# Kernel optimization log

Hardware: AMD Instinct MI355X
Metric: run time of the kernel (lower is better)

Reference implementation:

```python
import jax, jax.numpy as jnp
import numpy as np
from jax import lax

D_MODEL = 1024
FFN = 4096
CHUNK = 256
TTT_LR = 0.01
KSIZE = 5


def setup_inputs() -> dict:
    key = jax.random.key(0)
    ks = jax.random.split(key, 7)
    B, T = 2, 4096
    x = jax.random.normal(ks[0], (B, T, D_MODEL), dtype=jnp.float32)
    ttt_target = jax.random.normal(ks[1], (B, T, D_MODEL), dtype=jnp.float32)
    w_gate_up = jax.random.normal(ks[2], (2 * FFN, D_MODEL), dtype=jnp.float32) * 0.02
    w_down = jax.random.normal(ks[3], (D_MODEL, FFN), dtype=jnp.float32) * 0.02
    ttt_proj = jax.random.normal(ks[4], (D_MODEL, D_MODEL), dtype=jnp.float32) * 0.02
    conv_w = jax.random.normal(ks[5], (D_MODEL, 1, KSIZE), dtype=jnp.float32) * 0.02
    conv_b = jax.random.normal(ks[6], (D_MODEL,), dtype=jnp.float32) * 0.02
    return {"x": x, "ttt_target": ttt_target, "w_gate_up": w_gate_up,
            "w_down": w_down, "ttt_proj": ttt_proj, "conv_w": conv_w, "conv_b": conv_b}


def _pad_and_chunk(a, chunk):
    B, T, D = a.shape
    pad = (-T) % chunk
    if pad:
        a = jnp.pad(a, ((0, 0), (0, pad), (0, 0)))
    return a.reshape(B, -1, chunk, D)


def reference(x, ttt_target, w_gate_up, w_down, ttt_proj, conv_w, conv_b):
    B, T, D = x.shape
    # SwiGLU up path
    gate_up = jnp.einsum('btd,fd->btf', x, w_gate_up)  # (B,T,2F)
    gate, up = jnp.split(gate_up, 2, axis=-1)
    h = jax.nn.silu(gate) * up  # (B,T,F)
    # causal depthwise conv on ttt_target (torch pads K-1 both sides then slices [:T])
    t_ncl = ttt_target.transpose(0, 2, 1)  # (B,D,T)
    t = lax.conv_general_dilated(
        t_ncl, conv_w, window_strides=(1,), padding=[(KSIZE - 1, 0)],
        dimension_numbers=('NCH', 'OIH', 'NCH'), feature_group_count=D)
    t = (t + conv_b[None, :, None]).transpose(0, 2, 1)  # (B,T,D)
    # chunk
    h_c = _pad_and_chunk(h, CHUNK)  # (B,nc,C,F)
    t_c = _pad_and_chunk(t, CHUNK)  # (B,nc,C,D)
    nc = h_c.shape[1]
    if nc > 1:
        t_proj = jnp.einsum('btcd,ed->btce', t_c[:, :-1], ttt_proj)  # (B,nc-1,C,D)
        d_down = jnp.einsum('btch,btcd->btdh', h_c[:, :-1], t_proj)  # (B,nc-1,D,F)
    else:
        d_down = jnp.zeros((B, 0, D, FFN), dtype=h.dtype)
    w_orig = jnp.broadcast_to(w_down[None, None], (B, 1, D, FFN))
    w_all = jnp.concatenate([w_orig, d_down * jnp.float32(TTT_LR)], axis=1)
    w_adapted = jnp.cumsum(w_all, axis=1)  # (B,nc,D,F)
    out = jnp.einsum('btdh,btch->btcd', w_adapted, h_c)  # (B,nc,C,D)
    return out.reshape(B, -1, D)[:, :T]
```

## Files before the change

kernel.cpp:

```cpp
#include <hip/hip_runtime.h>
#include <hip/hip_bf16.h>
#include <stdint.h>

typedef unsigned short ushort_t;
typedef __bf16 bf16x8 __attribute__((ext_vector_type(8)));
typedef float f32x16 __attribute__((ext_vector_type(16)));

#define BM 128
#define BN 128
#define BK 64

__device__ inline float b2f(ushort_t u) {
    unsigned int x = ((unsigned int)u) << 16;
    float f; __builtin_memcpy(&f, &x, 4); return f;
}
__device__ inline ushort_t f2b(float f) {
    unsigned int x; __builtin_memcpy(&x, &f, 4);
    unsigned int r = (x + 0x7FFFu + ((x >> 16) & 1u)) >> 16;
    return (ushort_t)r;
}
__device__ inline void stage16(const ushort_t* g, ushort_t* s) {
    __builtin_amdgcn_global_load_lds((const __attribute__((address_space(1))) void*)g,
                                     (__attribute__((address_space(3))) void*)s, 16, 0, 0);
}
__device__ inline int swz(int r) { return (r & 7) ^ ((r >> 3) & 3); }
__device__ inline void stage_tile(const ushort_t* G, int ld, int k0, ushort_t* S, int tid) {
#pragma unroll
    for (int t = 0; t < 4; ++t) {
        int e = tid + t * 256;
        int row = e >> 3;
        int sw = ((e & 7) ^ swz(row)) * 8;
        stage16(G + (long long)row * ld + k0 + sw, &S[e * 8]);
    }
}
__device__ inline bf16x8 ldfrag(const ushort_t* S, int r, int c) {
    return *(const bf16x8*)&S[r * BK + ((c ^ swz(r)) * 8)];
}
__device__ inline void tile_decode(int& m0, int& n0) {
    const int nx = gridDim.x;
    int lin = blockIdx.y * nx + blockIdx.x;
    if ((nx & 7) == 0) {
        int q = nx >> 3;
        int k = lin & 7, s = lin >> 3;
        n0 = (k * q + s % q) * BN;
        m0 = (s / q) * BM;
    } else {
        m0 = blockIdx.y * BM;
        n0 = blockIdx.x * BN;
    }
}


#define SBAR() __builtin_amdgcn_sched_barrier(0)
#define BARRIER() do { SBAR(); __builtin_amdgcn_s_barrier(); SBAR(); } while (0)
#define WAITV(N) asm volatile("s_waitcnt vmcnt(" #N ")" ::: "memory")

__device__ inline int sw2(int r) { return ((r) & 3) ^ ((r >> 3) & 3); }

__device__ inline void stage_half(const ushort_t* G, int ldg, int kElem,
                                  ushort_t* Sbuf, int tid) {
#pragma unroll
    for (int i2 = 0; i2 < 2; ++i2) {
        int s = tid + i2 * 512;
        int r = s >> 2, q = s & 3;
        int c = q ^ sw2(r);
        stage16(G + (long long)r * ldg + kElem + c * 8, Sbuf + s * 8);
    }
}
__device__ inline void stage_halfA(const ushort_t* G, int ldg, ushort_t* Sbuf, int tid) {
    int r = tid >> 2, q = tid & 3;
    int c = q ^ sw2(r);
    stage16(G + (long long)r * ldg + c * 8, Sbuf + tid * 8);
}
__device__ inline int frag_off(int r, int c) {
    return r * 32 + ((c ^ sw2(r)) & 3) * 8;
}

__device__ __forceinline__ void gemm256_core(const ushort_t* __restrict__ Ag, int lda,
                                             const ushort_t* __restrict__ Bg, int ldb,
                                             int K, ushort_t* smem, int tid,
                                             int wr, int wc, int l32, int hl,
                                             f32x16 (&acc)[4][2]) {
    const int NH = K >> 5;
    ushort_t* Ab0 = smem;
    ushort_t* Bb0 = smem + 32768;

    int oa[4][2], ob[2][2];
#pragma unroll
    for (int m2 = 0; m2 < 4; ++m2)
#pragma unroll
        for (int k2 = 0; k2 < 2; ++k2)
            oa[m2][k2] = frag_off(wr * 128 + m2 * 32 + l32, k2 * 2 + hl);
#pragma unroll
    for (int n2 = 0; n2 < 2; ++n2)
#pragma unroll
        for (int k2 = 0; k2 < 2; ++k2)
            ob[n2][k2] = frag_off(wc * 64 + n2 * 32 + l32, k2 * 2 + hl);

    stage_half(Ag, lda, 0,  Ab0,          tid);
    stage_half(Bg, ldb, 0,  Bb0,          tid);
    stage_half(Ag, lda, 32, Ab0 + 8192,   tid);
    stage_half(Bg, ldb, 32, Bb0 + 8192,   tid);
    stage_half(Ag, lda, 64, Ab0 + 16384,  tid);
    stage_half(Bg, ldb, 64, Bb0 + 16384,  tid);
    WAITV(8);
    BARRIER();

    int h = 0;
    for (; h < NH - 3; ++h) {
        ushort_t* cA = Ab0 + (h & 3) * 8192;
        ushort_t* cB = Bb0 + (h & 3) * 8192;
        int nb = (h + 3) & 3;
        stage_half(Ag, lda, (h + 3) << 5, Ab0 + nb * 8192, tid);
        stage_half(Bg, ldb, (h + 3) << 5, Bb0 + nb * 8192, tid);
        bf16x8 af_[4][2], bf_[2][2];
#pragma unroll
        for (int k2 = 0; k2 < 2; ++k2) {
#pragma unroll
            for (int m2 = 0; m2 < 4; ++m2)
                af_[m2][k2] = *(const bf16x8*)&cA[oa[m2][k2]];
#pragma unroll
            for (int n2 = 0; n2 < 2; ++n2)
                bf_[n2][k2] = *(const bf16x8*)&cB[ob[n2][k2]];
        }
        __builtin_amdgcn_s_setprio(1);
#pragma unroll
        for (int k2 = 0; k2 < 2; ++k2)
#pragma unroll
            for (int m2 = 0; m2 < 4; ++m2)
#pragma unroll
                for (int n2 = 0; n2 < 2; ++n2)
                    acc[m2][n2] = __builtin_amdgcn_mfma_f32_32x32x16_bf16(
                        af_[m2][k2], bf_[n2][k2], acc[m2][n2], 0, 0, 0);
        __builtin_amdgcn_s_setprio(0);
        WAITV(8);
        BARRIER();
    }
    for (; h < NH; ++h) {
        ushort_t* cA = Ab0 + (h & 3) * 8192;
        ushort_t* cB = Bb0 + (h & 3) * 8192;
        bf16x8 af_[4][2], bf_[2][2];
#pragma unroll
        for (int k2 = 0; k2 < 2; ++k2) {
#pragma unroll
            for (int m2 = 0; m2 < 4; ++m2)
                af_[m2][k2] = *(const bf16x8*)&cA[oa[m2][k2]];
#pragma unroll
            for (int n2 = 0; n2 < 2; ++n2)
                bf_[n2][k2] = *(const bf16x8*)&cB[ob[n2][k2]];
        }
        __builtin_amdgcn_s_setprio(1);
#pragma unroll
        for (int k2 = 0; k2 < 2; ++k2)
#pragma unroll
            for (int m2 = 0; m2 < 4; ++m2)
#pragma unroll
                for (int n2 = 0; n2 < 2; ++n2)
                    acc[m2][n2] = __builtin_amdgcn_mfma_f32_32x32x16_bf16(
                        af_[m2][k2], bf_[n2][k2], acc[m2][n2], 0, 0, 0);
        __builtin_amdgcn_s_setprio(0);
        if (h + 2 < NH) { WAITV(4); } else { WAITV(0); }
        BARRIER();
    }
}

__global__ __launch_bounds__(512, 2)
void k_gemm256_silu(const ushort_t* __restrict__ A, const ushort_t* __restrict__ Bp,
                    ushort_t* __restrict__ H) {
    extern __shared__ __attribute__((aligned(16))) ushort_t smem2[];
    const int tid = threadIdx.x;
    const int lane = tid & 63, l32 = lane & 31, hl = lane >> 5;
    const int wv = tid >> 6, wr = wv >> 2, wc = wv & 3;
    int lin = blockIdx.y * 32 + blockIdx.x;
    int k8 = lin & 7, s = lin >> 3;
    int n0 = (k8 * 4 + (s & 3)) * 256;
    int m0 = (s >> 2) * 256;
    const ushort_t* Ag = A + (long long)m0 * 1024;
    const ushort_t* Bg = Bp + (long long)n0 * 1024;
    f32x16 acc[4][2];
#pragma unroll
    for (int i = 0; i < 4; ++i) { acc[i][0] = (f32x16)(0.f); acc[i][1] = (f32x16)(0.f); }
    gemm256_core(Ag, 1024, Bg, 1024, 1024, smem2, tid, wr, wc, l32, hl, acc);
    const int hc = (n0 >> 1) + wc * 32 + l32;
#pragma unroll
    for (int mi = 0; mi < 4; ++mi)
#pragma unroll
        for (int reg = 0; reg < 16; ++reg) {
            int row = m0 + wr * 128 + mi * 32 + (reg & 3) + 8 * (reg >> 2) + 4 * hl;
            float g = acc[mi][0][reg], u = acc[mi][1][reg];
            float sg = g / (1.f + __expf(-g));
            H[(long long)row * 4096 + hc] = f2b(sg * u);
        }
}

__global__ __launch_bounds__(512, 2)
void k_gemm256_tri(const ushort_t* __restrict__ Hh, ushort_t* __restrict__ P) {
    extern __shared__ __attribute__((aligned(16))) ushort_t smem2[];
    const int tid = threadIdx.x;
    const int lane = tid & 63, l32 = lane & 31, hl = lane >> 5;
    const int wv = tid >> 6, wr = wv >> 2, wc = wv & 3;
    int pairIdx = (blockIdx.x & 7) * 30 + (blockIdx.x >> 3);
    const int bb = pairIdx / 120;
    int p = pairIdx % 120;
    int i = 1, rem = p;
    while (rem >= i) { rem -= i; ++i; }
    const int j = rem;
    const ushort_t* Ag = Hh + (long long)bb * 4096 * 4096 + (long long)(i * 256) * 4096;
    const ushort_t* Bg = Hh + (long long)bb * 4096 * 4096 + (long long)(j * 256) * 4096;
    f32x16 acc[4][2];
#pragma unroll
    for (int a = 0; a < 4; ++a) { acc[a][0] = (f32x16)(0.f); acc[a][1] = (f32x16)(0.f); }
    gemm256_core(Ag, 4096, Bg, 4096, 4096, smem2, tid, wr, wc, l32, hl, acc);
    ushort_t* Pp = P + (long long)bb * 4096 * 4096;
#pragma unroll
    for (int mi = 0; mi < 4; ++mi)
#pragma unroll
        for (int nj = 0; nj < 2; ++nj) {
            int col = j * 256 + wc * 64 + nj * 32 + l32;
#pragma unroll
            for (int reg = 0; reg < 16; ++reg) {
                int row = i * 256 + wr * 128 + mi * 32 + (reg & 3) + 8 * (reg >> 2) + 4 * hl;
                Pp[(long long)row * 4096 + col] = f2b(acc[mi][nj][reg]);
            }
        }
}

__global__ __launch_bounds__(512, 2)
void k_gemm256_out(const ushort_t* __restrict__ h, const ushort_t* __restrict__ wdown,
                   const ushort_t* __restrict__ P, const ushort_t* __restrict__ tpT,
                   float* __restrict__ out) {
    constexpr int T = 4096, D = 1024, F = 4096, C = 256, K1 = 4096;
    extern __shared__ __attribute__((aligned(16))) ushort_t smem2[];
    const int tid = threadIdx.x;
    const int lane = tid & 63, l32 = lane & 31, hl = lane >> 5;
    const int wv = tid >> 6, wr = wv >> 2, wc = wv & 3;

    const int bx = blockIdx.x;
    const int logical = (bx & 7) * 32 + (bx >> 3);
    const int z = logical >> 3, t = logical & 7;
    const int bb = z >> 4, ii = z & 15;
    const int m0 = (t >> 2) * 128, n0 = (t & 3) * 256;
    const int K = K1 + ii * C;
    const int NH = K >> 5;

    const ushort_t* hA = h + (long long)bb * T * F + (long long)(ii * C + m0) * F;
    const ushort_t* pA = P + (long long)bb * T * T + (long long)(ii * C + m0) * T;
    const ushort_t* wB = wdown + (long long)n0 * F;
    const ushort_t* tB = tpT + (long long)bb * D * T + (long long)n0 * T;

    ushort_t* Ab0 = smem2;
    ushort_t* Bb0 = smem2 + 16384;

    int oa[2][2], ob[2][2];
#pragma unroll
    for (int m2 = 0; m2 < 2; ++m2)
#pragma unroll
        for (int k2 = 0; k2 < 2; ++k2)
            oa[m2][k2] = frag_off(wr * 64 + m2 * 32 + l32, k2 * 2 + hl);
#pragma unroll
    for (int n2 = 0; n2 < 2; ++n2)
#pragma unroll
        for (int k2 = 0; k2 < 2; ++k2)
            ob[n2][k2] = frag_off(wc * 64 + n2 * 32 + l32, k2 * 2 + hl);

    f32x16 acc[2][2];
#pragma unroll
    for (int a = 0; a < 2; ++a)
#pragma unroll
        for (int c = 0; c < 2; ++c) acc[a][c] = (f32x16)(0.f);

    auto srcA = [&](int kE) { return kE < K1 ? hA + kE : pA + (kE - K1); };
    auto srcB = [&](int kE) { return kE < K1 ? wB + kE : tB + (kE - K1); };

    stage_halfA(srcA(0),  F, Ab0,         tid);
    stage_half (srcB(0),  F, 0, Bb0,      tid);
    stage_halfA(srcA(32), F, Ab0 + 4096,  tid);
    stage_half (srcB(32), F, 0, Bb0 + 8192, tid);
    stage_halfA(srcA(64), F, Ab0 + 8192,  tid);
    stage_half (srcB(64), F, 0, Bb0 + 16384, tid);
    WAITV(6);
    BARRIER();

    int hh = 0;
    for (; hh < NH - 3; ++hh) {
        ushort_t* cA = Ab0 + (hh & 3) * 4096;
        ushort_t* cB = Bb0 + (hh & 3) * 8192;
        int nb = (hh + 3) & 3;
        stage_halfA(srcA((hh + 3) << 5), F, Ab0 + nb * 4096, tid);
        stage_half (srcB((hh + 3) << 5), F, 0, Bb0 + nb * 8192, tid);
        bf16x8 af_[2][2], bf_[2][2];
#pragma unroll
        for (int k2 = 0; k2 < 2; ++k2) {
#pragma unroll
            for (int m2 = 0; m2 < 2; ++m2)
                af_[m2][k2] = *(const bf16x8*)&cA[oa[m2][k2]];
#pragma unroll
            for (int n2 = 0; n2 < 2; ++n2)
                bf_[n2][k2] = *(const bf16x8*)&cB[ob[n2][k2]];
        }
        __builtin_amdgcn_s_setprio(1);
#pragma unroll
        for (int k2 = 0; k2 < 2; ++k2)
#pragma unroll
            for (int m2 = 0; m2 < 2; ++m2)
#pragma unroll
                for (int n2 = 0; n2 < 2; ++n2)
                    acc[m2][n2] = __builtin_amdgcn_mfma_f32_32x32x16_bf16(
                        af_[m2][k2], bf_[n2][k2], acc[m2][n2], 0, 0, 0);
        __builtin_amdgcn_s_setprio(0);
        WAITV(6);
        BARRIER();
    }
    for (; hh < NH; ++hh) {
        ushort_t* cA = Ab0 + (hh & 3) * 4096;
        ushort_t* cB = Bb0 + (hh & 3) * 8192;
        bf16x8 af_[2][2], bf_[2][2];
#pragma unroll
        for (int k2 = 0; k2 < 2; ++k2) {
#pragma unroll
            for (int m2 = 0; m2 < 2; ++m2)
                af_[m2][k2] = *(const bf16x8*)&cA[oa[m2][k2]];
#pragma unroll
            for (int n2 = 0; n2 < 2; ++n2)
                bf_[n2][k2] = *(const bf16x8*)&cB[ob[n2][k2]];
        }
        __builtin_amdgcn_s_setprio(1);
#pragma unroll
        for (int k2 = 0; k2 < 2; ++k2)
#pragma unroll
            for (int m2 = 0; m2 < 2; ++m2)
#pragma unroll
                for (int n2 = 0; n2 < 2; ++n2)
                    acc[m2][n2] = __builtin_amdgcn_mfma_f32_32x32x16_bf16(
                        af_[m2][k2], bf_[n2][k2], acc[m2][n2], 0, 0, 0);
        __builtin_amdgcn_s_setprio(0);
        if (hh + 2 < NH) { WAITV(3); } else { WAITV(0); }
        BARRIER();
    }

    float* Op = out + (long long)bb * T * D + (long long)(ii * C) * D;
#pragma unroll
    for (int mi = 0; mi < 2; ++mi)
#pragma unroll
        for (int nj = 0; nj < 2; ++nj) {
            int col = n0 + wc * 64 + nj * 32 + l32;
#pragma unroll
            for (int reg = 0; reg < 16; ++reg) {
                int row = m0 + wr * 64 + mi * 32 + (reg & 3) + 8 * (reg >> 2) + 4 * hl;
                Op[(long long)row * D + col] = acc[mi][nj][reg];
            }
        }
}

__global__ void k_prep(const float* __restrict__ x, const float* __restrict__ wgu,
                       const float* __restrict__ proj, const float* __restrict__ wdown,
                       const float* __restrict__ tt, const float* __restrict__ cw,
                       const float* __restrict__ cb,
                       ushort_t* __restrict__ xb, ushort_t* __restrict__ gb,
                       ushort_t* __restrict__ pb, ushort_t* __restrict__ wb,
                       ushort_t* __restrict__ tb, int permW) {
    constexpr int T = 4096, D = 1024;
    int blk = blockIdx.x;
    if (blk < 21504) {
        int i = blk * 256 + threadIdx.x;
        const float* src; ushort_t* dst; int off; int dstoff;
        if (i < 2097152)      { src = x;     dst = xb; off = i; dstoff = off; }
        else if (i < 4194304) {
            src = wgu; dst = gb; off = i - 2097152;
            if (permW) {
                int r = off >> 8, cu = off & 255;
                int pr = (r < 4096) ? (((r >> 5) << 6) + (r & 31))
                                    : ((((r - 4096) >> 5) << 6) + 32 + ((r - 4096) & 31));
                dstoff = (pr << 8) + cu;
            } else dstoff = off;
        }
        else if (i < 4456448) { src = proj;  dst = pb; off = i - 4194304; dstoff = off; }
        else                  { src = wdown; dst = wb; off = i - 4456448; dstoff = off; }
        float4 v = ((const float4*)src)[off];
        ushort4 o; o.x = f2b(v.x); o.y = f2b(v.y); o.z = f2b(v.z); o.w = f2b(v.w);
        ((ushort4*)dst)[dstoff] = o;
    } else {
        int idx = (blk - 21504) * 256 + threadIdx.x;
        int d = idx & (D - 1);
        int tq = (idx >> 10) & (T / 4 - 1);
        int b = idx / (D * (T / 4));
        int t0 = tq * 4;
        const float* base = tt + (long long)b * T * D + d;
        float w0 = cw[d * 5 + 0], w1 = cw[d * 5 + 1], w2 = cw[d * 5 + 2],
              w3 = cw[d * 5 + 3], w4 = cw[d * 5 + 4];
        float bias = cb[d];
        float win[8];
#pragma unroll
        for (int m = 0; m < 8; ++m) {
            int ts = t0 - 4 + m;
            win[m] = (ts >= 0) ? base[(long long)ts * D] : 0.f;
        }
        ushort_t* op = tb + (long long)b * T * D + (long long)t0 * D + d;
#pragma unroll
        for (int r = 0; r < 4; ++r) {
            float a = bias + w0 * win[r] + w1 * win[r + 1] + w2 * win[r + 2]
                    + w3 * win[r + 3] + w4 * win[r + 4];
            op[(long long)r * D] = f2b(a);
        }
    }
}

__global__ __launch_bounds__(256, 4)
void k_gemm_nt(const ushort_t* __restrict__ A, const ushort_t* __restrict__ B,
               ushort_t* __restrict__ C, int K, int lda, int ldb, int ldc,
               long long sAb, long long sBb, long long sCb, float scale) {
    __shared__ __attribute__((aligned(16))) ushort_t sA[BM * BK];
    __shared__ __attribute__((aligned(16))) ushort_t sB[BN * BK];

    int m0, n0;
    tile_decode(m0, n0);
    const int bb = blockIdx.z;
    const ushort_t* Ab = A + bb * sAb + (long long)m0 * lda;
    const ushort_t* Bb = B + bb * sBb + (long long)n0 * ldb;

    const int tid = threadIdx.x;
    const int lane = tid & 63, l32 = lane & 31, half = lane >> 5;
    const int wave = tid >> 6;
    const int wm = (wave >> 1) * 64, wn = (wave & 1) * 64;

    f32x16 acc[2][2];
#pragma unroll
    for (int i = 0; i < 2; ++i)
#pragma unroll
        for (int j = 0; j < 2; ++j) acc[i][j] = (f32x16)(0.f);

    for (int k0 = 0; k0 < K; k0 += BK) {
        __syncthreads();
        stage_tile(Ab, lda, k0, sA, tid);
        stage_tile(Bb, ldb, k0, sB, tid);
        __syncthreads();
#pragma unroll
        for (int ks = 0; ks < 4; ++ks) {
            bf16x8 af[2], bfr[2];
#pragma unroll
            for (int mi = 0; mi < 2; ++mi)
                af[mi] = ldfrag(sA, wm + mi * 32 + l32, ks * 2 + half);
#pragma unroll
            for (int nj = 0; nj < 2; ++nj)
                bfr[nj] = ldfrag(sB, wn + nj * 32 + l32, ks * 2 + half);
#pragma unroll
            for (int mi = 0; mi < 2; ++mi)
#pragma unroll
                for (int nj = 0; nj < 2; ++nj)
                    acc[mi][nj] = __builtin_amdgcn_mfma_f32_32x32x16_bf16(af[mi], bfr[nj], acc[mi][nj], 0, 0, 0);
        }
    }

    ushort_t* Cp = C + bb * sCb;
#pragma unroll
    for (int mi = 0; mi < 2; ++mi)
#pragma unroll
        for (int nj = 0; nj < 2; ++nj) {
            int col = n0 + wn + nj * 32 + l32;
#pragma unroll
            for (int reg = 0; reg < 16; ++reg) {
                int row = m0 + wm + mi * 32 + (reg & 3) + 8 * (reg >> 2) + 4 * half;
                Cp[(long long)row * ldc + col] = f2b(acc[mi][nj][reg] * scale);
            }
        }
}

__global__ __launch_bounds__(256)
void k_gemm_silu(const ushort_t* __restrict__ A, const ushort_t* __restrict__ Bg,
                 const ushort_t* __restrict__ Bu, ushort_t* __restrict__ H,
                 int K, int lda, int ldb, int ldh) {
    __shared__ __attribute__((aligned(16))) ushort_t sA[BM * BK];
    __shared__ __attribute__((aligned(16))) ushort_t sBg[BN * BK];
    __shared__ __attribute__((aligned(16))) ushort_t sBu[BN * BK];

    int m0, n0;
    tile_decode(m0, n0);
    const ushort_t* Ab = A + (long long)m0 * lda;
    const ushort_t* Bgb = Bg + (long long)n0 * ldb;
    const ushort_t* Bub = Bu + (long long)n0 * ldb;

    const int tid = threadIdx.x;
    const int lane = tid & 63, l32 = lane & 31, half = lane >> 5;
    const int wave = tid >> 6;
    const int wm = (wave >> 1) * 64, wn = (wave & 1) * 64;

    f32x16 ag[2][2], au[2][2];
#pragma unroll
    for (int i = 0; i < 2; ++i)
#pragma unroll
        for (int j = 0; j < 2; ++j) { ag[i][j] = (f32x16)(0.f); au[i][j] = (f32x16)(0.f); }

    for (int k0 = 0; k0 < K; k0 += BK) {
        __syncthreads();
        stage_tile(Ab, lda, k0, sA, tid);
        stage_tile(Bgb, ldb, k0, sBg, tid);
        stage_tile(Bub, ldb, k0, sBu, tid);
        __syncthreads();
#pragma unroll
        for (int ks = 0; ks < 4; ++ks) {
            bf16x8 af[2], bg[2], bu[2];
#pragma unroll
            for (int mi = 0; mi < 2; ++mi)
                af[mi] = ldfrag(sA, wm + mi * 32 + l32, ks * 2 + half);
#pragma unroll
            for (int nj = 0; nj < 2; ++nj) {
                bg[nj] = ldfrag(sBg, wn + nj * 32 + l32, ks * 2 + half);
                bu[nj] = ldfrag(sBu, wn + nj * 32 + l32, ks * 2 + half);
            }
#pragma unroll
            for (int mi = 0; mi < 2; ++mi)
#pragma unroll
                for (int nj = 0; nj < 2; ++nj) {
                    ag[mi][nj] = __builtin_amdgcn_mfma_f32_32x32x16_bf16(af[mi], bg[nj], ag[mi][nj], 0, 0, 0);
                    au[mi][nj] = __builtin_amdgcn_mfma_f32_32x32x16_bf16(af[mi], bu[nj], au[mi][nj], 0, 0, 0);
                }
        }
    }

#pragma unroll
    for (int mi = 0; mi < 2; ++mi)
#pragma unroll
        for (int nj = 0; nj < 2; ++nj) {
            int col = n0 + wn + nj * 32 + l32;
#pragma unroll
            for (int reg = 0; reg < 16; ++reg) {
                int row = m0 + wm + mi * 32 + (reg & 3) + 8 * (reg >> 2) + 4 * half;
                float g = ag[mi][nj][reg], u = au[mi][nj][reg];
                float s = g / (1.f + __expf(-g));
                H[(long long)row * ldh + col] = f2b(s * u);
            }
        }
}

__global__ __launch_bounds__(256, 4)
void k_gemm_tri(const ushort_t* __restrict__ H, ushort_t* __restrict__ P,
                int K, int ldh, int ldp, long long sHb, long long sPb) {
    __shared__ __attribute__((aligned(16))) ushort_t sA[BM * BK];
    __shared__ __attribute__((aligned(16))) ushort_t sB[BN * BK];

    const int lin = blockIdx.x;
    const int g = lin >> 5, w = lin & 31;
    const int xk = w & 7, t = w >> 3;
    int pairIdx = g * 8 + xk;
    const int bb = pairIdx / 120;
    int p = pairIdx % 120;
    int i = 1, rem = p;
    while (rem >= i) { rem -= i; ++i; }
    const int j = rem;
    const int m0 = (t >> 1) * BM, n0 = (t & 1) * BN;

    const ushort_t* Ab = H + bb * sHb + (long long)(i * 256 + m0) * ldh;
    const ushort_t* Bb = H + bb * sHb + (long long)(j * 256 + n0) * ldh;

    const int tid = threadIdx.x;
    const int lane = tid & 63, l32 = lane & 31, half = lane >> 5;
    const int wave = tid >> 6;
    const int wm = (wave >> 1) * 64, wn = (wave & 1) * 64;

    f32x16 acc[2][2];
#pragma unroll
    for (int a = 0; a < 2; ++a)
#pragma unroll
        for (int c = 0; c < 2; ++c) acc[a][c] = (f32x16)(0.f);

    for (int k0 = 0; k0 < K; k0 += BK) {
        __syncthreads();
        stage_tile(Ab, ldh, k0, sA, tid);
        stage_tile(Bb, ldh, k0, sB, tid);
        __syncthreads();
#pragma unroll
        for (int ks = 0; ks < 4; ++ks) {
            bf16x8 af[2], bfr[2];
#pragma unroll
            for (int mi = 0; mi < 2; ++mi)
                af[mi] = ldfrag(sA, wm + mi * 32 + l32, ks * 2 + half);
#pragma unroll
            for (int nj = 0; nj < 2; ++nj)
                bfr[nj] = ldfrag(sB, wn + nj * 32 + l32, ks * 2 + half);
#pragma unroll
            for (int mi = 0; mi < 2; ++mi)
#pragma unroll
                for (int nj = 0; nj < 2; ++nj)
                    acc[mi][nj] = __builtin_amdgcn_mfma_f32_32x32x16_bf16(af[mi], bfr[nj], acc[mi][nj], 0, 0, 0);
        }
    }

    ushort_t* Pp = P + bb * sPb;
#pragma unroll
    for (int mi = 0; mi < 2; ++mi)
#pragma unroll
        for (int nj = 0; nj < 2; ++nj) {
            int col = j * 256 + n0 + wn + nj * 32 + l32;
#pragma unroll
            for (int reg = 0; reg < 16; ++reg) {
                int row = i * 256 + m0 + wm + mi * 32 + (reg & 3) + 8 * (reg >> 2) + 4 * half;
                Pp[(long long)row * ldp + col] = f2b(acc[mi][nj][reg]);
            }
        }
}

__global__ __launch_bounds__(256, 4)
void k_gemm_out(const ushort_t* __restrict__ h, const ushort_t* __restrict__ wdown,
                const ushort_t* __restrict__ P, const ushort_t* __restrict__ tpT,
                float* __restrict__ out) {
    constexpr int T = 4096, D = 1024, F = 4096, C = 256, K1 = 4096;
    __shared__ __attribute__((aligned(16))) ushort_t sA[BM * BK];
    __shared__ __attribute__((aligned(16))) ushort_t sB[BN * BK];

    const int z = blockIdx.z, bb = z >> 4, ii = z & 15;
    const int K2 = ii * C;
    int m0, n0;
    tile_decode(m0, n0);

    const ushort_t* A1 = h + (long long)bb * T * F + (long long)(ii * C + m0) * F;
    const ushort_t* B1 = wdown + (long long)n0 * F;
    const ushort_t* A2 = P + (long long)bb * T * T + (long long)(ii * C + m0) * T;
    const ushort_t* B2 = tpT + (long long)bb * D * T + (long long)n0 * T;

    const int tid = threadIdx.x;
    const int lane = tid & 63, l32 = lane & 31, half = lane >> 5;
    const int wave = tid >> 6;
    const int wm = (wave >> 1) * 64, wn = (wave & 1) * 64;

    f32x16 acc[2][2];
#pragma unroll
    for (int i = 0; i < 2; ++i)
#pragma unroll
        for (int j = 0; j < 2; ++j) acc[i][j] = (f32x16)(0.f);

    const int K = K1 + K2;
    for (int k0 = 0; k0 < K; k0 += BK) {
        const ushort_t* As = (k0 < K1) ? A1 + k0 : A2 + (k0 - K1);
        const ushort_t* Bs = (k0 < K1) ? B1 + k0 : B2 + (k0 - K1);
        __syncthreads();
        stage_tile(As, 4096, 0, sA, tid);
        stage_tile(Bs, 4096, 0, sB, tid);
        __syncthreads();
#pragma unroll
        for (int ks = 0; ks < 4; ++ks) {
            bf16x8 af[2], bfr[2];
#pragma unroll
            for (int mi = 0; mi < 2; ++mi)
                af[mi] = ldfrag(sA, wm + mi * 32 + l32, ks * 2 + half);
#pragma unroll
            for (int nj = 0; nj < 2; ++nj)
                bfr[nj] = ldfrag(sB, wn + nj * 32 + l32, ks * 2 + half);
#pragma unroll
            for (int mi = 0; mi < 2; ++mi)
#pragma unroll
                for (int nj = 0; nj < 2; ++nj)
                    acc[mi][nj] = __builtin_amdgcn_mfma_f32_32x32x16_bf16(af[mi], bfr[nj], acc[mi][nj], 0, 0, 0);
        }
    }

    float* Op = out + (long long)bb * T * D + (long long)ii * C * D;
#pragma unroll
    for (int mi = 0; mi < 2; ++mi)
#pragma unroll
        for (int nj = 0; nj < 2; ++nj) {
            int col = n0 + wn + nj * 32 + l32;
#pragma unroll
            for (int reg = 0; reg < 16; ++reg) {
                int row = m0 + wm + mi * 32 + (reg & 3) + 8 * (reg >> 2) + 4 * half;
                Op[(long long)row * D + col] = acc[mi][nj][reg];
            }
        }
}

static int g_big = -1;

extern "C" void kernel_launch(void* const* d_in, const int* in_sizes, int n_in,
                              void* d_out, int out_size, void* d_ws, size_t ws_size,
                              hipStream_t stream) {
    const float* x         = (const float*)d_in[0];
    const float* ttt_tgt   = (const float*)d_in[1];
    const float* w_gate_up = (const float*)d_in[2];
    const float* w_down    = (const float*)d_in[3];
    const float* ttt_proj  = (const float*)d_in[4];
    const float* conv_w    = (const float*)d_in[5];
    const float* conv_b    = (const float*)d_in[6];
    float* out = (float*)d_out;
    (void)in_sizes; (void)n_in; (void)out_size; (void)ws_size;

    constexpr int Bb = 2, T = 4096, D = 1024, F = 4096, C = 256;
    constexpr float LR = 0.01f;

    if (g_big < 0) {
        hipError_t e1 = hipFuncSetAttribute((const void*)k_gemm256_silu,
                                            hipFuncAttributeMaxDynamicSharedMemorySize, 131072);
        hipError_t e2 = hipFuncSetAttribute((const void*)k_gemm256_tri,
                                            hipFuncAttributeMaxDynamicSharedMemorySize, 131072);
        hipError_t e3 = hipFuncSetAttribute((const void*)k_gemm256_out,
                                            hipFuncAttributeMaxDynamicSharedMemorySize, 98304);
        g_big = (e1 == hipSuccess && e2 == hipSuccess && e3 == hipSuccess) ? 1 : 0;
    }

    char* ws = (char*)d_ws;
    ushort_t* x_bf     = (ushort_t*)(ws);
    ushort_t* wgu_bf   = (ushort_t*)(ws + 16777216LL);
    ushort_t* t_bf     = (ushort_t*)(ws + 2 * 16777216LL);
    ushort_t* P        = (ushort_t*)(ws);
    ushort_t* proj_bf  = (ushort_t*)(ws + 67108864LL);
    ushort_t* wdown_bf = (ushort_t*)(ws + 67108864LL + 2097152LL);
    ushort_t* tpT      = (ushort_t*)(ws + 67108864LL + 2097152LL + 8388608LL);
    ushort_t* h        = (ushort_t*)(ws + 67108864LL + 2097152LL + 8388608LL + 16777216LL);

    k_prep<<<21504 + 8192, 256, 0, stream>>>(x, w_gate_up, ttt_proj, w_down,
                                             ttt_tgt, conv_w, conv_b,
                                             x_bf, wgu_bf, proj_bf, wdown_bf, t_bf, g_big);

    k_gemm_nt<<<dim3(T / BN, D / BM, Bb), 256, 0, stream>>>(
        proj_bf, t_bf, tpT, D, D, D, T,
        0, (long long)T * D, (long long)D * T, LR);

    if (g_big) {
        k_gemm256_silu<<<dim3(32, 32, 1), 512, 131072, stream>>>(x_bf, wgu_bf, h);
    } else {
        k_gemm_silu<<<dim3(F / BN, (Bb * T) / BM, 1), 256, 0, stream>>>(
            x_bf, wgu_bf, wgu_bf + (long long)F * D, h, D, D, D, F);
    }

    if (g_big) {
        k_gemm256_tri<<<dim3(240, 1, 1), 512, 131072, stream>>>(h, P);
    } else {
        k_gemm_tri<<<dim3(960, 1, 1), 256, 0, stream>>>(
            h, P, F, F, T, (long long)T * F, (long long)T * T);
    }

    if (g_big) {
        k_gemm256_out<<<dim3(256, 1, 1), 512, 98304, stream>>>(h, wdown_bf, P, tpT, out);
    } else {
        k_gemm_out<<<dim3(D / BN, C / BM, Bb * 16), 256, 0, stream>>>(
            h, wdown_bf, P, tpT, out);
    }
}
```

Measured before the change: 563.7 us.

## Use 16-wave blocks for big GEMMs and split-K balance the output GEMM

The 256x256 silu and triangular GEMM kernels now run 1024 threads (16 waves), each wave owning a 64x64 sub-tile. They use a double-buffered two-half staging pipeline over BK=64 in place of the 4-stage ring of 32-wide K slices. The output GEMM pairs chunk i with chunk 15-i and splits each chunk's K range in half, accumulating into a zeroed output with atomicAdd, to even out the triangular work across blocks. This adds a memset, fp32 atomic traffic and nondeterministic summation order, and the 1024-thread path is enabled only when the attribute query confirms support.

Measured after the change: 608.5 us. 8.0% more time.

```diff
diff --git a/kernel.cpp b/kernel.cpp
--- a/kernel.cpp
+++ b/kernel.cpp
@@ -57,67 +57,75 @@
 
 __device__ inline int sw2(int r) { return ((r) & 3) ^ ((r >> 3) & 3); }
 
-__device__ inline void stage_half(const ushort_t* G, int ldg, int kElem,
-                                  ushort_t* Sbuf, int tid) {
+__device__ inline void stage1k(const ushort_t* G, int ldg, int kElem,
+                               ushort_t* Sbuf, int tid) {
+    int r = tid >> 2, q = tid & 3;
+    int c = q ^ sw2(r);
+    stage16(G + (long long)r * ldg + kElem + c * 8, Sbuf + tid * 8);
+}
+__device__ inline void ostageA(const ushort_t* G, ushort_t* Sbuf, int tid) {
+    int r = tid >> 2, q = tid & 3;
+    stage16(G + (long long)r * 4096 + (q ^ sw2(r)) * 8, Sbuf + tid * 8);
+}
+__device__ inline void ostageB(const ushort_t* G, ushort_t* Sbuf, int tid) {
 #pragma unroll
     for (int i2 = 0; i2 < 2; ++i2) {
         int s = tid + i2 * 512;
         int r = s >> 2, q = s & 3;
-        int c = q ^ sw2(r);
-        stage16(G + (long long)r * ldg + kElem + c * 8, Sbuf + s * 8);
-    }
-}
-__device__ inline void stage_halfA(const ushort_t* G, int ldg, ushort_t* Sbuf, int tid) {
-    int r = tid >> 2, q = tid & 3;
-    int c = q ^ sw2(r);
-    stage16(G + (long long)r * ldg + c * 8, Sbuf + tid * 8);
+        stage16(G + (long long)r * 4096 + (q ^ sw2(r)) * 8, Sbuf + s * 8);
+    }
 }
 __device__ inline int frag_off(int r, int c) {
     return r * 32 + ((c ^ sw2(r)) & 3) * 8;
 }
 
-__device__ __forceinline__ void gemm256_core(const ushort_t* __restrict__ Ag, int lda,
-                                             const ushort_t* __restrict__ Bg, int ldb,
-                                             int K, ushort_t* smem, int tid,
-                                             int wr, int wc, int l32, int hl,
-                                             f32x16 (&acc)[4][2]) {
-    const int NH = K >> 5;
-    ushort_t* Ab0 = smem;
-    ushort_t* Bb0 = smem + 32768;
-
-    int oa[4][2], ob[2][2];
-#pragma unroll
-    for (int m2 = 0; m2 < 4; ++m2)
+__device__ __forceinline__ void gemm256w16_core(const ushort_t* __restrict__ Ag, int lda,
+                                                const ushort_t* __restrict__ Bg, int ldb,
+                                                int K, ushort_t* smem, int tid,
+                                                int wr, int wc, int l32, int hl,
+                                                f32x16 (&acc)[2][2]) {
+    ushort_t* A0s = smem;
+    ushort_t* A1s = smem + 16384;
+    ushort_t* B0s = smem + 32768;
+    ushort_t* B1s = smem + 49152;
+    const int NT = K >> 6;
+
+    int oa[2][2], ob[2][2];
+#pragma unroll
+    for (int m2 = 0; m2 < 2; ++m2)
 #pragma unroll
         for (int k2 = 0; k2 < 2; ++k2)
-            oa[m2][k2] = frag_off(wr * 128 + m2 * 32 + l32, k2 * 2 + hl);
+            oa[m2][k2] = frag_off(wr * 64 + m2 * 32 + l32, k2 * 2 + hl);
 #pragma unroll
     for (int n2 = 0; n2 < 2; ++n2)
 #pragma unroll
         for (int k2 = 0; k2 < 2; ++k2)
             ob[n2][k2] = frag_off(wc * 64 + n2 * 32 + l32, k2 * 2 + hl);
 
-    stage_half(Ag, lda, 0,  Ab0,          tid);
-    stage_half(Bg, ldb, 0,  Bb0,          tid);
-    stage_half(Ag, lda, 32, Ab0 + 8192,   tid);
-    stage_half(Bg, ldb, 32, Bb0 + 8192,   tid);
-    stage_half(Ag, lda, 64, Ab0 + 16384,  tid);
-    stage_half(Bg, ldb, 64, Bb0 + 16384,  tid);
-    WAITV(8);
+    stage1k(Ag, lda, 0,  A0s,        tid);
+    stage1k(Bg, ldb, 0,  B0s,        tid);
+    stage1k(Ag, lda, 32, A0s + 8192, tid);
+    stage1k(Bg, ldb, 32, B0s + 8192, tid);
+    stage1k(Ag, lda, 64, A1s,        tid);
+    stage1k(Bg, ldb, 64, B1s,        tid);
+    WAITV(4);
     BARRIER();
 
-    int h = 0;
-    for (; h < NH - 3; ++h) {
-        ushort_t* cA = Ab0 + (h & 3) * 8192;
-        ushort_t* cB = Bb0 + (h & 3) * 8192;
-        int nb = (h + 3) & 3;
-        stage_half(Ag, lda, (h + 3) << 5, Ab0 + nb * 8192, tid);
-        stage_half(Bg, ldb, (h + 3) << 5, Bb0 + nb * 8192, tid);
-        bf16x8 af_[4][2], bf_[2][2];
+    for (int kt = 0; kt < NT; ++kt) {
+        ushort_t* cA = (kt & 1) ? A1s : A0s;
+        ushort_t* cB = (kt & 1) ? B1s : B0s;
+        ushort_t* nA = (kt & 1) ? A0s : A1s;
+        ushort_t* nB = (kt & 1) ? B0s : B1s;
+        const bool h1 = (kt + 1 < NT), h2 = (kt + 2 < NT);
+        bf16x8 af_[2][2], bf_[2][2];
+        if (h1) {
+            stage1k(Ag, lda, ((kt + 1) << 6) + 32, nA + 8192, tid);
+            stage1k(Bg, ldb, ((kt + 1) << 6) + 32, nB + 8192, tid);
+        }
 #pragma unroll
         for (int k2 = 0; k2 < 2; ++k2) {
 #pragma unroll
-            for (int m2 = 0; m2 < 4; ++m2)
+            for (int m2 = 0; m2 < 2; ++m2)
                 af_[m2][k2] = *(const bf16x8*)&cA[oa[m2][k2]];
 #pragma unroll
             for (int n2 = 0; n2 < 2; ++n2)
@@ -127,44 +135,43 @@
 #pragma unroll
         for (int k2 = 0; k2 < 2; ++k2)
 #pragma unroll
-            for (int m2 = 0; m2 < 4; ++m2)
+            for (int m2 = 0; m2 < 2; ++m2)
 #pragma unroll
                 for (int n2 = 0; n2 < 2; ++n2)
                     acc[m2][n2] = __builtin_amdgcn_mfma_f32_32x32x16_bf16(
                         af_[m2][k2], bf_[n2][k2], acc[m2][n2], 0, 0, 0);
         __builtin_amdgcn_s_setprio(0);
-        WAITV(8);
+        if (h1) { WAITV(4); } else { WAITV(0); }
         BARRIER();
-    }
-    for (; h < NH; ++h) {
-        ushort_t* cA = Ab0 + (h & 3) * 8192;
-        ushort_t* cB = Bb0 + (h & 3) * 8192;
-        bf16x8 af_[4][2], bf_[2][2];
+        if (h2) {
+            stage1k(Ag, lda, (kt + 2) << 6, cA, tid);
+            stage1k(Bg, ldb, (kt + 2) << 6, cB, tid);
+        }
 #pragma unroll
         for (int k2 = 0; k2 < 2; ++k2) {
 #pragma unroll
-            for (int m2 = 0; m2 < 4; ++m2)
-                af_[m2][k2] = *(const bf16x8*)&cA[oa[m2][k2]];
+            for (int m2 = 0; m2 < 2; ++m2)
+                af_[m2][k2] = *(const bf16x8*)&cA[oa[m2][k2] + 8192];
 #pragma unroll
             for (int n2 = 0; n2 < 2; ++n2)
-                bf_[n2][k2] = *(const bf16x8*)&cB[ob[n2][k2]];
+                bf_[n2][k2] = *(const bf16x8*)&cB[ob[n2][k2] + 8192];
         }
         __builtin_amdgcn_s_setprio(1);
 #pragma unroll
         for (int k2 = 0; k2 < 2; ++k2)
 #pragma unroll
-            for (int m2 = 0; m2 < 4; ++m2)
+            for (int m2 = 0; m2 < 2; ++m2)
 #pragma unroll
                 for (int n2 = 0; n2 < 2; ++n2)
                     acc[m2][n2] = __builtin_amdgcn_mfma_f32_32x32x16_bf16(
                         af_[m2][k2], bf_[n2][k2], acc[m2][n2], 0, 0, 0);
         __builtin_amdgcn_s_setprio(0);
-        if (h + 2 < NH) { WAITV(4); } else { WAITV(0); }
+        if (h1) { if (h2) { WAITV(4); } else { WAITV(2); } } else { WAITV(0); }
         BARRIER();
     }
 }
 
-__global__ __launch_bounds__(512, 2)
+__global__ __launch_bounds__(1024, 4)
 void k_gemm256_silu(const ushort_t* __restrict__ A, const ushort_t* __restrict__ Bp,
                     ushort_t* __restrict__ H) {
     extern __shared__ __attribute__((aligned(16))) ushort_t smem2[];
@@ -177,23 +184,23 @@
     int m0 = (s >> 2) * 256;
     const ushort_t* Ag = A + (long long)m0 * 1024;
     const ushort_t* Bg = Bp + (long long)n0 * 1024;
-    f32x16 acc[4][2];
-#pragma unroll
-    for (int i = 0; i < 4; ++i) { acc[i][0] = (f32x16)(0.f); acc[i][1] = (f32x16)(0.f); }
-    gemm256_core(Ag, 1024, Bg, 1024, 1024, smem2, tid, wr, wc, l32, hl, acc);
+    f32x16 acc[2][2];
+#pragma unroll
+    for (int i = 0; i < 2; ++i) { acc[i][0] = (f32x16)(0.f); acc[i][1] = (f32x16)(0.f); }
+    gemm256w16_core(Ag, 1024, Bg, 1024, 1024, smem2, tid, wr, wc, l32, hl, acc);
     const int hc = (n0 >> 1) + wc * 32 + l32;
 #pragma unroll
-    for (int mi = 0; mi < 4; ++mi)
+    for (int mi = 0; mi < 2; ++mi)
 #pragma unroll
         for (int reg = 0; reg < 16; ++reg) {
-            int row = m0 + wr * 128 + mi * 32 + (reg & 3) + 8 * (reg >> 2) + 4 * hl;
+            int row = m0 + wr * 64 + mi * 32 + (reg & 3) + 8 * (reg >> 2) + 4 * hl;
             float g = acc[mi][0][reg], u = acc[mi][1][reg];
             float sg = g / (1.f + __expf(-g));
             H[(long long)row * 4096 + hc] = f2b(sg * u);
         }
 }
 
-__global__ __launch_bounds__(512, 2)
+__global__ __launch_bounds__(1024, 4)
 void k_gemm256_tri(const ushort_t* __restrict__ Hh, ushort_t* __restrict__ P) {
     extern __shared__ __attribute__((aligned(16))) ushort_t smem2[];
     const int tid = threadIdx.x;
@@ -207,19 +214,19 @@
     const int j = rem;
     const ushort_t* Ag = Hh + (long long)bb * 4096 * 4096 + (long long)(i * 256) * 4096;
     const ushort_t* Bg = Hh + (long long)bb * 4096 * 4096 + (long long)(j * 256) * 4096;
-    f32x16 acc[4][2];
-#pragma unroll
-    for (int a = 0; a < 4; ++a) { acc[a][0] = (f32x16)(0.f); acc[a][1] = (f32x16)(0.f); }
-    gemm256_core(Ag, 4096, Bg, 4096, 4096, smem2, tid, wr, wc, l32, hl, acc);
+    f32x16 acc[2][2];
+#pragma unroll
+    for (int a = 0; a < 2; ++a) { acc[a][0] = (f32x16)(0.f); acc[a][1] = (f32x16)(0.f); }
+    gemm256w16_core(Ag, 4096, Bg, 4096, 4096, smem2, tid, wr, wc, l32, hl, acc);
     ushort_t* Pp = P + (long long)bb * 4096 * 4096;
 #pragma unroll
-    for (int mi = 0; mi < 4; ++mi)
+    for (int mi = 0; mi < 2; ++mi)
 #pragma unroll
         for (int nj = 0; nj < 2; ++nj) {
             int col = j * 256 + wc * 64 + nj * 32 + l32;
 #pragma unroll
             for (int reg = 0; reg < 16; ++reg) {
-                int row = i * 256 + wr * 128 + mi * 32 + (reg & 3) + 8 * (reg >> 2) + 4 * hl;
+                int row = i * 256 + wr * 64 + mi * 32 + (reg & 3) + 8 * (reg >> 2) + 4 * hl;
                 Pp[(long long)row * 4096 + col] = f2b(acc[mi][nj][reg]);
             }
         }
@@ -236,20 +243,17 @@
     const int wv = tid >> 6, wr = wv >> 2, wc = wv & 3;
 
     const int bx = blockIdx.x;
-    const int logical = (bx & 7) * 32 + (bx >> 3);
-    const int z = logical >> 3, t = logical & 7;
-    const int bb = z >> 4, ii = z & 15;
+    const int xcd = bx & 7, s = bx >> 3;
+    const int pl = s >> 4, halfSel = (s >> 3) & 1, t = s & 7;
+    const int p = 2 * xcd + pl;
+    const int bb = p >> 3, iiL = p & 7;
+    const int ii0 = halfSel ? (15 - iiL) : iiL;
     const int m0 = (t >> 2) * 128, n0 = (t & 3) * 256;
-    const int K = K1 + ii * C;
-    const int NH = K >> 5;
-
-    const ushort_t* hA = h + (long long)bb * T * F + (long long)(ii * C + m0) * F;
-    const ushort_t* pA = P + (long long)bb * T * T + (long long)(ii * C + m0) * T;
-    const ushort_t* wB = wdown + (long long)n0 * F;
-    const ushort_t* tB = tpT + (long long)bb * D * T + (long long)n0 * T;
-
-    ushort_t* Ab0 = smem2;
-    ushort_t* Bb0 = smem2 + 16384;
+
+    ushort_t* A0s = smem2;
+    ushort_t* A1s = smem2 + 8192;
+    ushort_t* B0s = smem2 + 16384;
+    ushort_t* B1s = smem2 + 32768;
 
     int oa[2][2], ob[2][2];
 #pragma unroll
@@ -263,93 +267,110 @@
         for (int k2 = 0; k2 < 2; ++k2)
             ob[n2][k2] = frag_off(wc * 64 + n2 * 32 + l32, k2 * 2 + hl);
 
-    f32x16 acc[2][2];
-#pragma unroll
-    for (int a = 0; a < 2; ++a)
-#pragma unroll
-        for (int c = 0; c < 2; ++c) acc[a][c] = (f32x16)(0.f);
-
-    auto srcA = [&](int kE) { return kE < K1 ? hA + kE : pA + (kE - K1); };
-    auto srcB = [&](int kE) { return kE < K1 ? wB + kE : tB + (kE - K1); };
-
-    stage_halfA(srcA(0),  F, Ab0,         tid);
-    stage_half (srcB(0),  F, 0, Bb0,      tid);
-    stage_halfA(srcA(32), F, Ab0 + 4096,  tid);
-    stage_half (srcB(32), F, 0, Bb0 + 8192, tid);
-    stage_halfA(srcA(64), F, Ab0 + 8192,  tid);
-    stage_half (srcB(64), F, 0, Bb0 + 16384, tid);
-    WAITV(6);
-    BARRIER();
-
-    int hh = 0;
-    for (; hh < NH - 3; ++hh) {
-        ushort_t* cA = Ab0 + (hh & 3) * 4096;
-        ushort_t* cB = Bb0 + (hh & 3) * 8192;
-        int nb = (hh + 3) & 3;
-        stage_halfA(srcA((hh + 3) << 5), F, Ab0 + nb * 4096, tid);
-        stage_half (srcB((hh + 3) << 5), F, 0, Bb0 + nb * 8192, tid);
-        bf16x8 af_[2][2], bf_[2][2];
-#pragma unroll
-        for (int k2 = 0; k2 < 2; ++k2) {
-#pragma unroll
-            for (int m2 = 0; m2 < 2; ++m2)
-                af_[m2][k2] = *(const bf16x8*)&cA[oa[m2][k2]];
-#pragma unroll
-            for (int n2 = 0; n2 < 2; ++n2)
-                bf_[n2][k2] = *(const bf16x8*)&cB[ob[n2][k2]];
-        }
-        __builtin_amdgcn_s_setprio(1);
-#pragma unroll
-        for (int k2 = 0; k2 < 2; ++k2)
-#pragma unroll
-            for (int m2 = 0; m2 < 2; ++m2)
-#pragma unroll
-                for (int n2 = 0; n2 < 2; ++n2)
-                    acc[m2][n2] = __builtin_amdgcn_mfma_f32_32x32x16_bf16(
-                        af_[m2][k2], bf_[n2][k2], acc[m2][n2], 0, 0, 0);
-        __builtin_amdgcn_s_setprio(0);
+#pragma unroll 1
+    for (int it = 0; it < 2; ++it) {
+        const int ii = it ? (15 - ii0) : ii0;
+        const int NT = 64 + 4 * ii;
+        const int NTh = NT >> 1;
+        const int ktBeg = it ? NTh : 0;
+        const int NTs = it ? (NT - NTh) : NTh;
+
+        const ushort_t* hA = h + (long long)bb * T * F + (long long)(ii * C + m0) * F;
+        const ushort_t* pA = P + (long long)bb * T * T + (long long)(ii * C + m0) * T;
+        const ushort_t* wB = wdown + (long long)n0 * F;
+        const ushort_t* tB = tpT + (long long)bb * D * T + (long long)n0 * T;
+        auto srcA = [&](int kE) { return kE < K1 ? hA + kE : pA + (kE - K1); };
+        auto srcB = [&](int kE) { return kE < K1 ? wB + kE : tB + (kE - K1); };
+
+        f32x16 acc[2][2];
+#pragma unroll
+        for (int a = 0; a < 2; ++a)
+#pragma unroll
+            for (int c = 0; c < 2; ++c) acc[a][c] = (f32x16)(0.f);
+
+        const int kE0 = ktBeg << 6;
+        ostageA(srcA(kE0),      A0s,        tid);
+        ostageB(srcB(kE0),      B0s,        tid);
+        ostageA(srcA(kE0 + 32), A0s + 4096, tid);
+        ostageB(srcB(kE0 + 32), B0s + 8192, tid);
+        ostageA(srcA(kE0 + 64), A1s,        tid);
+        ostageB(srcB(kE0 + 64), B1s,        tid);
         WAITV(6);
         BARRIER();
-    }
-    for (; hh < NH; ++hh) {
-        ushort_t* cA = Ab0 + (hh & 3) * 4096;
-        ushort_t* cB = Bb0 + (hh & 3) * 8192;
-        bf16x8 af_[2][2], bf_[2][2];
-#pragma unroll
-        for (int k2 = 0; k2 < 2; ++k2) {
-#pragma unroll
-            for (int m2 = 0; m2 < 2; ++m2)
-                af_[m2][k2] = *(const bf16x8*)&cA[oa[m2][k2]];
-#pragma unroll
-            for (int n2 = 0; n2 < 2; ++n2)
-                bf_[n2][k2] = *(const bf16x8*)&cB[ob[n2][k2]];
-        }
-        __builtin_amdgcn_s_setprio(1);
-#pragma unroll
-        for (int k2 = 0; k2 < 2; ++k2)
-#pragma unroll
-            for (int m2 = 0; m2 < 2; ++m2)
+
+        for (int kt = 0; kt < NTs; ++kt) {
+            ushort_t* cA = (kt & 1) ? A1s : A0s;
+            ushort_t* cB = (kt & 1) ? B1s : B0s;
+            ushort_t* nA = (kt & 1) ? A0s : A1s;
+            ushort_t* nB = (kt & 1) ? B0s : B1s;
+            const bool h1 = (kt + 1 < NTs), h2 = (kt + 2 < NTs);
+            const int kE1 = (ktBeg + kt + 1) << 6, kE2 = (ktBeg + kt + 2) << 6;
+            bf16x8 af_[2][2], bf_[2][2];
+            if (h1) {
+                ostageA(srcA(kE1 + 32), nA + 4096, tid);
+                ostageB(srcB(kE1 + 32), nB + 8192, tid);
+            }
+#pragma unroll
+            for (int k2 = 0; k2 < 2; ++k2) {
+#pragma unroll
+                for (int m2 = 0; m2 < 2; ++m2)
+                    af_[m2][k2] = *(const bf16x8*)&cA[oa[m2][k2]];
 #pragma unroll
                 for (int n2 = 0; n2 < 2; ++n2)
-                    acc[m2][n2] = __builtin_amdgcn_mfma_f32_32x32x16_bf16(
-                        af_[m2][k2], bf_[n2][k2], acc[m2][n2], 0, 0, 0);
-        __builtin_amdgcn_s_setprio(0);
-        if (hh + 2 < NH) { WAITV(3); } else { WAITV(0); }
-        BARRIER();
-    }
-
-    float* Op = out + (long long)bb * T * D + (long long)(ii * C) * D;
-#pragma unroll
-    for (int mi = 0; mi < 2; ++mi)
-#pragma unroll
-        for (int nj = 0; nj < 2; ++nj) {
-            int col = n0 + wc * 64 + nj * 32 + l32;
-#pragma unroll
-            for (int reg = 0; reg < 16; ++reg) {
-                int row = m0 + wr * 64 + mi * 32 + (reg & 3) + 8 * (reg >> 2) + 4 * hl;
-                Op[(long long)row * D + col] = acc[mi][nj][reg];
-            }
-        }
+                    bf_[n2][k2] = *(const bf16x8*)&cB[ob[n2][k2]];
+            }
+            __builtin_amdgcn_s_setprio(1);
+#pragma unroll
+            for (int k2 = 0; k2 < 2; ++k2)
+#pragma unroll
+                for (int m2 = 0; m2 < 2; ++m2)
+#pragma unroll
+                    for (int n2 = 0; n2 < 2; ++n2)
+                        acc[m2][n2] = __builtin_amdgcn_mfma_f32_32x32x16_bf16(
+                            af_[m2][k2], bf_[n2][k2], acc[m2][n2], 0, 0, 0);
+            __builtin_amdgcn_s_setprio(0);
+            if (h1) { WAITV(6); } else { WAITV(0); }
+            BARRIER();
+            if (h2) {
+                ostageA(srcA(kE2), cA, tid);
+                ostageB(srcB(kE2), cB, tid);
+            }
+#pragma unroll
+            for (int k2 = 0; k2 < 2; ++k2) {
+#pragma unroll
+                for (int m2 = 0; m2 < 2; ++m2)
+                    af_[m2][k2] = *(const bf16x8*)&cA[oa[m2][k2] + 4096];
+#pragma unroll
+                for (int n2 = 0; n2 < 2; ++n2)
+                    bf_[n2][k2] = *(const bf16x8*)&cB[ob[n2][k2] + 8192];
+            }
+            __builtin_amdgcn_s_setprio(1);
+#pragma unroll
+            for (int k2 = 0; k2 < 2; ++k2)
+#pragma unroll
+                for (int m2 = 0; m2 < 2; ++m2)
+#pragma unroll
+                    for (int n2 = 0; n2 < 2; ++n2)
+                        acc[m2][n2] = __builtin_amdgcn_mfma_f32_32x32x16_bf16(
+                            af_[m2][k2], bf_[n2][k2], acc[m2][n2], 0, 0, 0);
+            __builtin_amdgcn_s_setprio(0);
+            if (h2) { WAITV(6); } else { if (h1) { WAITV(3); } else { WAITV(0); } }
+            BARRIER();
+        }
+
+        float* Op = out + (long long)bb * T * D + (long long)(ii * C) * D;
+#pragma unroll
+        for (int mi = 0; mi < 2; ++mi)
+#pragma unroll
+            for (int nj = 0; nj < 2; ++nj) {
+                int col = n0 + wc * 64 + nj * 32 + l32;
+#pragma unroll
+                for (int reg = 0; reg < 16; ++reg) {
+                    int row = m0 + wr * 64 + mi * 32 + (reg & 3) + 8 * (reg >> 2) + 4 * hl;
+                    atomicAdd(&Op[(long long)row * D + col], acc[mi][nj][reg]);
+                }
+            }
+    }
 }
 
 __global__ void k_prep(const float* __restrict__ x, const float* __restrict__ wgu,
@@ -680,7 +701,7 @@
     const float* conv_w    = (const float*)d_in[5];
     const float* conv_b    = (const float*)d_in[6];
     float* out = (float*)d_out;
-    (void)in_sizes; (void)n_in; (void)out_size; (void)ws_size;
+    (void)in_sizes; (void)n_in; (void)ws_size;
 
     constexpr int Bb = 2, T = 4096, D = 1024, F = 4096, C = 256;
     constexpr float LR = 0.01f;
@@ -692,7 +713,12 @@
                                             hipFuncAttributeMaxDynamicSharedMemorySize, 131072);
         hipError_t e3 = hipFuncSetAttribute((const void*)k_gemm256_out,
                                             hipFuncAttributeMaxDynamicSharedMemorySize, 98304);
-        g_big = (e1 == hipSuccess && e2 == hipSuccess && e3 == hipSuccess) ? 1 : 0;
+        hipFuncAttributes a1{}, a2{};
+        hipError_t e4 = hipFuncGetAttributes(&a1, (const void*)k_gemm256_silu);
+        hipError_t e5 = hipFuncGetAttributes(&a2, (const void*)k_gemm256_tri);
+        bool big1024 = (e4 == hipSuccess && a1.maxThreadsPerBlock >= 1024) &&
+                       (e5 == hipSuccess && a2.maxThreadsPerBlock >= 1024);
+        g_big = (e1 == hipSuccess && e2 == hipSuccess && e3 == hipSuccess && big1024) ? 1 : 0;
     }
 
     char* ws = (char*)d_ws;
@@ -705,6 +731,8 @@
     ushort_t* tpT      = (ushort_t*)(ws + 67108864LL + 2097152LL + 8388608LL);
     ushort_t* h        = (ushort_t*)(ws + 67108864LL + 2097152LL + 8388608LL + 16777216LL);
 
+    if (g_big) hipMemsetAsync(out, 0, (size_t)out_size, stream);
+
     k_prep<<<21504 + 8192, 256, 0, stream>>>(x, w_gate_up, ttt_proj, w_down,
                                              ttt_tgt, conv_w, conv_b,
                                              x_bf, wgu_bf, proj_bf, wdown_bf, t_bf, g_big);
@@ -714,14 +742,14 @@
         0, (long long)T * D, (long long)D * T, LR);
 
     if (g_big) {
-        k_gemm256_silu<<<dim3(32, 32, 1), 512, 131072, stream>>>(x_bf, wgu_bf, h);
+        k_gemm256_silu<<<dim3(32, 32, 1), 1024, 131072, stream>>>(x_bf, wgu_bf, h);
     } else {
         k_gemm_silu<<<dim3(F / BN, (Bb * T) / BM, 1), 256, 0, stream>>>(
             x_bf, wgu_bf, wgu_bf + (long long)F * D, h, D, D, D, F);
     }
 
     if (g_big) {
-        k_gemm256_tri<<<dim3(240, 1, 1), 512, 131072, stream>>>(h, P);
+        k_gemm256_tri<<<dim3(240, 1, 1), 1024, 131072, stream>>>(h, P);
     } else {
         k_gemm_tri<<<dim3(960, 1, 1), 256, 0, stream>>>(
             h, P, F, F, T, (long long)T * F, (long long)T * T);
```
